# Kernel tuning notes

Measured on AMD Instinct MI355X. Metric: run time of the kernel, lower is better.

Reference implementation:

```python
import jax, jax.numpy as jnp
import numpy as np

BINS = 8
EPS = 1e-12  # torch F.normalize default eps


def _pairwise_scores(matf):
    # torch: input1[a,b]=matf[b]; transpose(0,1)->matf[a]; transpose(-2,-1)->matf[a]^T [M,F]
    # matmul with input1[a,b]=matf[b] -> scores[a,b] = matf[a]^T @ matf[b], shape [M,M]
    bs, F, M = matf.shape
    s = jnp.einsum('afm,bfn->abmn', matf, matf)  # [bs, bs, M, M]
    return s.reshape(bs * bs, M * M)


def _histc_rows(x, bins):
    # torch.histc semantics with min=max=0: range = [row.min(), row.max()],
    # values == max land in the last bin.
    mn = jnp.min(x, axis=1, keepdims=True)
    mx = jnp.max(x, axis=1, keepdims=True)
    denom = jnp.where(mx > mn, mx - mn, jnp.ones_like(mx))
    idx = jnp.clip(jnp.floor((x - mn) / denom * bins).astype(jnp.int32), 0, bins - 1)
    nbs = x.shape[0]
    flat = (idx + (jnp.arange(nbs, dtype=jnp.int32) * bins)[:, None]).ravel()
    h = jnp.zeros(nbs * bins, dtype=x.dtype).at[flat].add(1.0)
    return h.reshape(nbs, bins)


def _l2_normalize(h):
    n = jnp.linalg.norm(h, axis=-1, keepdims=True)
    return h / jnp.maximum(n, EPS)


def setup_inputs() -> dict:
    key = jax.random.key(0)
    k1, k2 = jax.random.split(key)
    bs, F, M = 64, 256, 128
    matf1 = jax.random.normal(k1, (bs, F, M), dtype=jnp.float32)
    matf2 = jax.random.normal(k2, (bs, F, M), dtype=jnp.float32)
    return {"matf1": matf1, "matf2": matf2}


def reference(matf1, matf2):
    # scores are .detach()ed in the original; stop_gradient for faithfulness
    scores1 = jax.lax.stop_gradient(_pairwise_scores(matf1))  # [nbs, M*M]
    scores2 = jax.lax.stop_gradient(_pairwise_scores(matf2))
    h1 = _l2_normalize(_histc_rows(scores1, BINS))  # [nbs, 8]
    h2 = _l2_normalize(_histc_rows(scores2, BINS))
    return jnp.concatenate([h1, h2], axis=-1)  # [nbs, 16]
```

## Files before the change

### kernel.cpp

```cpp
#include <hip/hip_runtime.h>
#include <math.h>

#define BS 64
#define F  256
#define M  128
#define MF (M * F)
#define NTILE 528

typedef unsigned short u16;
typedef _Float16 f16x8 __attribute__((ext_vector_type(8)));
typedef float    f32x16 __attribute__((ext_vector_type(16)));

__global__ __launch_bounds__(256) void convert_f16_kernel(
    const float* __restrict__ m1, const float* __restrict__ m2,
    u16* __restrict__ hT)
{
    __shared__ float tile[64 * M];
    const int mat = blockIdx.x >> 6;
    const int b   = blockIdx.x & 63;
    const int f0  = blockIdx.y * 64;
    const float* src = (mat == 0 ? m1 : m2) + (size_t)b * MF + (size_t)f0 * M;
    const int tid = threadIdx.x;

    const float4* g = (const float4*)src;
    float4* s = (float4*)tile;
    #pragma unroll
    for (int i = 0; i < 8; ++i)
        s[tid + i * 256] = g[tid + i * 256];
    __syncthreads();

    const size_t obase = ((size_t)(mat * BS + b) * 32 + (f0 >> 3)) * 1024;
    #pragma unroll
    for (int it = 0; it < 4; ++it) {
        const int idx = it * 256 + tid;
        const int f8l = idx >> 7;
        const int m   = idx & 127;
        u16 hh[8] __attribute__((aligned(16)));
        #pragma unroll
        for (int j = 0; j < 8; ++j) {
            const float x = tile[(f8l * 8 + j) * M + m];
            const _Float16 h = (_Float16)x;
            hh[j] = __builtin_bit_cast(u16, h);
        }
        *(uint4*)&hT[obase + (size_t)idx * 8] = *(const uint4*)hh;
    }
}


#define SLOAD(S) {                                    \
    const u16* sp = srcp + (S) * 8192;                \
    sr0 = *(const uint4*)(sp);                        \
    sr1 = *(const uint4*)(sp + 1024);                 \
    sr2 = *(const uint4*)(sp + 2048);                 \
    sr3 = *(const uint4*)(sp + 3072);                 \
    sr4 = *(const uint4*)(sp + 4096);                 \
    sr5 = *(const uint4*)(sp + 5120);                 \
    sr6 = *(const uint4*)(sp + 6144);                 \
    sr7 = *(const uint4*)(sp + 7168);                 \
}

#define SWRITE(BUF) {                                 \
    u16* dp = &lds[dstb + (BUF)];                     \
    *(uint4*)(dp)        = sr0;                       \
    *(uint4*)(dp + 1024) = sr1;                       \
    *(uint4*)(dp + 2048) = sr2;                       \
    *(uint4*)(dp + 3072) = sr3;                       \
    *(uint4*)(dp + 4096) = sr4;                       \
    *(uint4*)(dp + 5120) = sr5;                       \
    *(uint4*)(dp + 6144) = sr6;                       \
    *(uint4*)(dp + 7168) = sr7;                       \
}

#define MFMA_SLICE(BUF) {                                                                             \
    __builtin_amdgcn_s_setprio(1);                                                                    \
    _Pragma("unroll")                                                                                 \
    for (int ITl = 0; ITl < 2; ++ITl) {                                                               \
        _Pragma("unroll")                                                                             \
        for (int kk = 0; kk < 2; ++kk) {                                                              \
            const int base = (BUF) + ITl * 4096 + kk * 2048;                                          \
            f16x8 af[4], bf[2];                                                                       \
            _Pragma("unroll")                                                                         \
            for (int t = 0; t < 4; ++t)                                                               \
                af[t] = *(const f16x8*)&lds[base + aoffW + t * 256];                                  \
            bf[0] = *(const f16x8*)&lds[base + boffW];                                                \
            bf[1] = *(const f16x8*)&lds[base + boffW + 256];                                          \
            _Pragma("unroll")                                                                         \
            for (int ti = 0; ti < 4; ++ti) {                                                          \
                acc[ti][0] = __builtin_amdgcn_mfma_f32_32x32x16_f16(af[ti], bf[0], acc[ti][0], 0, 0, 0); \
                acc[ti][1] = __builtin_amdgcn_mfma_f32_32x32x16_f16(af[ti], bf[1], acc[ti][1], 0, 0, 0); \
            }                                                                                         \
        }                                                                                             \
    }                                                                                                 \
    __builtin_amdgcn_s_setprio(0);                                                                    \
}

__global__ __launch_bounds__(512, 2) void gram_hist_mfma(
    const u16* __restrict__ hT, float* __restrict__ out)
{
    __shared__ u16 lds[4 * 2 * 8192];
    __shared__ float smin[8], smax[8];
    __shared__ int hist[4][8];

    const int tid  = threadIdx.x;
    const int lane = tid & 63;
    const int w    = tid >> 6;

    if (tid < 32) hist[tid >> 3][tid & 7] = 0;

    int x = blockIdx.x;
    x = (x & 7) * 66 + (x >> 3);
    int tt = x, ta = 0, cnt = 32;
    while (tt >= cnt) { tt -= cnt; ++ta; cnt = 32 - ta; }
    const int tb  = ta + tt;
    const int mat = blockIdx.y;

    const int m  = w >> 1;
    const int c  = w & 1;
    const int l31   = lane & 31;
    const int lhalf = lane >> 5;

    const int srow = tid >> 7;
    const int tl   = tid & 127;
    const int rsel = (srow < 2) ? (2 * ta + srow) : (2 * tb + (srow - 2));
    const u16* srcp = hT + (size_t)(mat * BS + rsel) * MF + tl * 8;
    const int dstb = srow * 16384 + tl * 8;

    const int aoffW = (m >> 1) * 16384 + lhalf * 1024 + l31 * 8;
    const int boffW = (2 + (m & 1)) * 16384 + lhalf * 1024 + c * 512 + l31 * 8;

    f32x16 acc[4][2];
    #pragma unroll
    for (int ti = 0; ti < 4; ++ti)
        #pragma unroll
        for (int u = 0; u < 2; ++u)
            #pragma unroll
            for (int r = 0; r < 16; ++r) acc[ti][u][r] = 0.0f;

    uint4 sr0, sr1, sr2, sr3, sr4, sr5, sr6, sr7;

    SLOAD(0); SWRITE(0);
    __syncthreads();

    SLOAD(1);
    MFMA_SLICE(0);
    __builtin_amdgcn_sched_barrier(0);
    SWRITE(8192);
    __syncthreads();

    SLOAD(2);
    MFMA_SLICE(8192);
    __builtin_amdgcn_sched_barrier(0);
    SWRITE(0);
    __syncthreads();

    SLOAD(3);
    MFMA_SLICE(0);
    __builtin_amdgcn_sched_barrier(0);
    SWRITE(8192);
    __syncthreads();

    MFMA_SLICE(8192);

    float vmin = acc[0][0][0], vmax = vmin;
    #pragma unroll
    for (int ti = 0; ti < 4; ++ti)
        #pragma unroll
        for (int u = 0; u < 2; ++u)
            #pragma unroll
            for (int r = 0; r < 16; ++r) {
                vmin = fminf(vmin, acc[ti][u][r]);
                vmax = fmaxf(vmax, acc[ti][u][r]);
            }
    #pragma unroll
    for (int off = 1; off < 64; off <<= 1) {
        vmin = fminf(vmin, __shfl_xor(vmin, off, 64));
        vmax = fmaxf(vmax, __shfl_xor(vmax, off, 64));
    }
    if (lane == 0) { smin[w] = vmin; smax[w] = vmax; }
    __syncthreads();
    const float pmn = fminf(smin[m * 2], smin[m * 2 + 1]);
    const float pmx = fmaxf(smax[m * 2], smax[m * 2 + 1]);
    const float denom = (pmx > pmn) ? (pmx - pmn) : 1.0f;
    const float scale = 8.0f / denom;
    const float bias  = -pmn * scale;

    unsigned w0 = 0, w1 = 0;
    #pragma unroll
    for (int ti = 0; ti < 4; ++ti)
        #pragma unroll
        for (int u = 0; u < 2; ++u)
            #pragma unroll
            for (int r = 0; r < 16; ++r) {
                const float t = fmaf(acc[ti][u][r], scale, bias);
                int k = (int)t;
                k = k > 7 ? 7 : k;
                const unsigned inc = 1u << ((k & 3) * 8);
                if (k < 4) w0 += inc; else w1 += inc;
            }
    unsigned e0 = (w0 & 0xFFu)         | (((w0 >> 8)  & 0xFFu) << 16);
    unsigned e1 = ((w0 >> 16) & 0xFFu) | (((w0 >> 24) & 0xFFu) << 16);
    unsigned e2 = (w1 & 0xFFu)         | (((w1 >> 8)  & 0xFFu) << 16);
    unsigned e3 = ((w1 >> 16) & 0xFFu) | (((w1 >> 24) & 0xFFu) << 16);
    #pragma unroll
    for (int off = 32; off > 0; off >>= 1) {
        e0 += __shfl_down(e0, off, 64);
        e1 += __shfl_down(e1, off, 64);
        e2 += __shfl_down(e2, off, 64);
        e3 += __shfl_down(e3, off, 64);
    }
    if (lane == 0) {
        atomicAdd(&hist[m][0], (int)(e0 & 0xFFFFu)); atomicAdd(&hist[m][1], (int)(e0 >> 16));
        atomicAdd(&hist[m][2], (int)(e1 & 0xFFFFu)); atomicAdd(&hist[m][3], (int)(e1 >> 16));
        atomicAdd(&hist[m][4], (int)(e2 & 0xFFFFu)); atomicAdd(&hist[m][5], (int)(e2 >> 16));
        atomicAdd(&hist[m][6], (int)(e3 & 0xFFFFu)); atomicAdd(&hist[m][7], (int)(e3 >> 16));
    }
    __syncthreads();

    if (c == 0 && lane < 8) {
        float ss = 0.0f;
        #pragma unroll
        for (int k = 0; k < 8; ++k) {
            const float cc = (float)hist[m][k];
            ss += cc * cc;
        }
        const float nrm = fmaxf(sqrtf(ss), 1e-12f);
        const float v = (float)hist[m][lane] / nrm;
        const int A = 2 * ta + (m >> 1);
        const int B = 2 * tb + (m & 1);
        out[((size_t)A * BS + B) * 16 + mat * 8 + lane] = v;
        if (A != B)
            out[((size_t)B * BS + A) * 16 + mat * 8 + lane] = v;
    }
}

extern "C" void kernel_launch(void* const* d_in, const int* in_sizes, int n_in,
                              void* d_out, int out_size, void* d_ws, size_t ws_size,
                              hipStream_t stream) {
    const float* m1 = (const float*)d_in[0];
    const float* m2 = (const float*)d_in[1];
    float* out = (float*)d_out;

    u16* hT = (u16*)d_ws;

    convert_f16_kernel<<<dim3(128, 4), 256, 0, stream>>>(m1, m2, hT);
    gram_hist_mfma<<<dim3(NTILE, 2), 512, 0, stream>>>(hT, out);
}
```

Before: 127.9 us.

## Use direct global-to-LDS loads with 1024-thread blocks and finer K pipeline

Replaces the register-staged global loads and LDS writes with global_load_lds direct-to-LDS transfers. Doubles the block to 16 waves, each computing a 64x64 sub-tile. Halves the K-slice size and uses an 8-stage double-buffered loop. The grid is flattened so the XCD id picks the matrix and tile group. This cuts register pressure and staging instructions, at the cost of more barriers per block and smaller per-wave MFMA work.

```diff
diff --git a/kernel.cpp b/kernel.cpp
--- a/kernel.cpp
+++ b/kernel.cpp
@@ -5,11 +5,14 @@
 #define F  256
 #define M  128
 #define MF (M * F)
-#define NTILE 528
+#define NT2 528
 
 typedef unsigned short u16;
 typedef _Float16 f16x8 __attribute__((ext_vector_type(8)));
 typedef float    f32x16 __attribute__((ext_vector_type(16)));
+
+typedef const __attribute__((address_space(1))) void gas_t;
+typedef __attribute__((address_space(3))) void las_t;
 
 __global__ __launch_bounds__(256) void convert_f16_kernel(
     const float* __restrict__ m1, const float* __restrict__ m2,
@@ -47,58 +50,38 @@
 }
 
 
-#define SLOAD(S) {                                    \
-    const u16* sp = srcp + (S) * 8192;                \
-    sr0 = *(const uint4*)(sp);                        \
-    sr1 = *(const uint4*)(sp + 1024);                 \
-    sr2 = *(const uint4*)(sp + 2048);                 \
-    sr3 = *(const uint4*)(sp + 3072);                 \
-    sr4 = *(const uint4*)(sp + 4096);                 \
-    sr5 = *(const uint4*)(sp + 5120);                 \
-    sr6 = *(const uint4*)(sp + 6144);                 \
-    sr7 = *(const uint4*)(sp + 7168);                 \
-}
-
-#define SWRITE(BUF) {                                 \
-    u16* dp = &lds[dstb + (BUF)];                     \
-    *(uint4*)(dp)        = sr0;                       \
-    *(uint4*)(dp + 1024) = sr1;                       \
-    *(uint4*)(dp + 2048) = sr2;                       \
-    *(uint4*)(dp + 3072) = sr3;                       \
-    *(uint4*)(dp + 4096) = sr4;                       \
-    *(uint4*)(dp + 5120) = sr5;                       \
-    *(uint4*)(dp + 6144) = sr6;                       \
-    *(uint4*)(dp + 7168) = sr7;                       \
-}
-
-#define MFMA_SLICE(BUF) {                                                                             \
-    __builtin_amdgcn_s_setprio(1);                                                                    \
-    _Pragma("unroll")                                                                                 \
-    for (int ITl = 0; ITl < 2; ++ITl) {                                                               \
-        _Pragma("unroll")                                                                             \
-        for (int kk = 0; kk < 2; ++kk) {                                                              \
-            const int base = (BUF) + ITl * 4096 + kk * 2048;                                          \
-            f16x8 af[4], bf[2];                                                                       \
-            _Pragma("unroll")                                                                         \
-            for (int t = 0; t < 4; ++t)                                                               \
-                af[t] = *(const f16x8*)&lds[base + aoffW + t * 256];                                  \
-            bf[0] = *(const f16x8*)&lds[base + boffW];                                                \
-            bf[1] = *(const f16x8*)&lds[base + boffW + 256];                                          \
-            _Pragma("unroll")                                                                         \
-            for (int ti = 0; ti < 4; ++ti) {                                                          \
-                acc[ti][0] = __builtin_amdgcn_mfma_f32_32x32x16_f16(af[ti], bf[0], acc[ti][0], 0, 0, 0); \
-                acc[ti][1] = __builtin_amdgcn_mfma_f32_32x32x16_f16(af[ti], bf[1], acc[ti][1], 0, 0, 0); \
-            }                                                                                         \
-        }                                                                                             \
-    }                                                                                                 \
-    __builtin_amdgcn_s_setprio(0);                                                                    \
-}
-
-__global__ __launch_bounds__(512, 2) void gram_hist_mfma(
+#define GLOAD(S, BUF) {                                                       \
+    const u16* g0 = srow + (S) * 4096 + j0 * 512 + lane * 8;                  \
+    const u16* g1 = srow + (S) * 4096 + j1 * 512 + lane * 8;                  \
+    __builtin_amdgcn_global_load_lds((gas_t*)g0,                              \
+        (las_t*)&lds[ldst0 + (BUF)], 16, 0, 0);                               \
+    __builtin_amdgcn_global_load_lds((gas_t*)g1,                              \
+        (las_t*)&lds[ldst1 + (BUF)], 16, 0, 0);                               \
+}
+
+#define MFMA_SLICE(BUF) {                                                     \
+    __builtin_amdgcn_s_setprio(1);                                            \
+    _Pragma("unroll")                                                         \
+    for (int kk = 0; kk < 2; ++kk) {                                          \
+        const int ab = ra * 8192 + (BUF) + kk * 2048 + aoffb;                 \
+        const int bb = rb * 8192 + (BUF) + kk * 2048 + boffb;                 \
+        const f16x8 a0 = *(const f16x8*)&lds[ab];                             \
+        const f16x8 a1 = *(const f16x8*)&lds[ab + 256];                       \
+        const f16x8 b0 = *(const f16x8*)&lds[bb];                             \
+        const f16x8 b1 = *(const f16x8*)&lds[bb + 256];                       \
+        acc[0][0] = __builtin_amdgcn_mfma_f32_32x32x16_f16(a0, b0, acc[0][0], 0, 0, 0); \
+        acc[0][1] = __builtin_amdgcn_mfma_f32_32x32x16_f16(a0, b1, acc[0][1], 0, 0, 0); \
+        acc[1][0] = __builtin_amdgcn_mfma_f32_32x32x16_f16(a1, b0, acc[1][0], 0, 0, 0); \
+        acc[1][1] = __builtin_amdgcn_mfma_f32_32x32x16_f16(a1, b1, acc[1][1], 0, 0, 0); \
+    }                                                                         \
+    __builtin_amdgcn_s_setprio(0);                                            \
+}
+
+__global__ __launch_bounds__(1024, 4) void gram_hist_mfma(
     const u16* __restrict__ hT, float* __restrict__ out)
 {
-    __shared__ u16 lds[4 * 2 * 8192];
-    __shared__ float smin[8], smax[8];
+    __shared__ u16 lds[4 * 2 * 4096];
+    __shared__ float smin[16], smax[16];
     __shared__ int hist[4][8];
 
     const int tid  = threadIdx.x;
@@ -107,69 +90,63 @@
 
     if (tid < 32) hist[tid >> 3][tid & 7] = 0;
 
-    int x = blockIdx.x;
-    x = (x & 7) * 66 + (x >> 3);
-    int tt = x, ta = 0, cnt = 32;
-    while (tt >= cnt) { tt -= cnt; ++ta; cnt = 32 - ta; }
-    const int tb  = ta + tt;
-    const int mat = blockIdx.y;
-
-    const int m  = w >> 1;
-    const int c  = w & 1;
+    const int bid = blockIdx.x;
+    const int xcd = bid & 7;
+    const int mat = xcd >> 2;
+    int p = (xcd & 3) * 132 + (bid >> 3);
+    int ta = 0;
+    { int cnt = 32; while (p >= cnt) { p -= cnt; ++ta; cnt = 32 - ta; } }
+    const int tb = ta + p;
+
+    const int m  = w >> 2;
+    const int q  = w & 3;
+    const int qr = q >> 1;
+    const int qc = q & 1;
     const int l31   = lane & 31;
     const int lhalf = lane >> 5;
 
-    const int srow = tid >> 7;
-    const int tl   = tid & 127;
-    const int rsel = (srow < 2) ? (2 * ta + srow) : (2 * tb + (srow - 2));
-    const u16* srcp = hT + (size_t)(mat * BS + rsel) * MF + tl * 8;
-    const int dstb = srow * 16384 + tl * 8;
-
-    const int aoffW = (m >> 1) * 16384 + lhalf * 1024 + l31 * 8;
-    const int boffW = (2 + (m & 1)) * 16384 + lhalf * 1024 + c * 512 + l31 * 8;
-
-    f32x16 acc[4][2];
-    #pragma unroll
-    for (int ti = 0; ti < 4; ++ti)
+    const int k0  = w * 2;
+    const int r_s = k0 >> 3;
+    const int rowsel = (r_s < 2) ? (2 * ta + r_s) : (2 * tb + (r_s - 2));
+    const u16* srow = hT + (size_t)(mat * BS + rowsel) * MF;
+    const int j0 = k0 & 7, j1 = (k0 + 1) & 7;
+    const int ldst0 = r_s * 8192 + j0 * 512;
+    const int ldst1 = r_s * 8192 + j1 * 512;
+
+    const int ra = m >> 1;
+    const int rb = 2 + (m & 1);
+    const int aoffb = lhalf * 1024 + qr * 512 + l31 * 8;
+    const int boffb = lhalf * 1024 + qc * 512 + l31 * 8;
+
+    f32x16 acc[2][2];
+    #pragma unroll
+    for (int t = 0; t < 2; ++t)
         #pragma unroll
         for (int u = 0; u < 2; ++u)
             #pragma unroll
-            for (int r = 0; r < 16; ++r) acc[ti][u][r] = 0.0f;
-
-    uint4 sr0, sr1, sr2, sr3, sr4, sr5, sr6, sr7;
-
-    SLOAD(0); SWRITE(0);
-    __syncthreads();
-
-    SLOAD(1);
-    MFMA_SLICE(0);
-    __builtin_amdgcn_sched_barrier(0);
-    SWRITE(8192);
-    __syncthreads();
-
-    SLOAD(2);
-    MFMA_SLICE(8192);
-    __builtin_amdgcn_sched_barrier(0);
-    SWRITE(0);
-    __syncthreads();
-
-    SLOAD(3);
-    MFMA_SLICE(0);
-    __builtin_amdgcn_sched_barrier(0);
-    SWRITE(8192);
-    __syncthreads();
-
-    MFMA_SLICE(8192);
+            for (int r = 0; r < 16; ++r) acc[t][u][r] = 0.0f;
+
+    GLOAD(0, 0);
+    __syncthreads();
+
+    #pragma unroll
+    for (int s = 0; s < 8; ++s) {
+        const int cur = (s & 1) * 4096;
+        const int alt = cur ^ 4096;
+        if (s < 7) GLOAD(s + 1, alt);
+        MFMA_SLICE(cur);
+        __syncthreads();
+    }
 
     float vmin = acc[0][0][0], vmax = vmin;
     #pragma unroll
-    for (int ti = 0; ti < 4; ++ti)
+    for (int t = 0; t < 2; ++t)
         #pragma unroll
         for (int u = 0; u < 2; ++u)
             #pragma unroll
             for (int r = 0; r < 16; ++r) {
-                vmin = fminf(vmin, acc[ti][u][r]);
-                vmax = fmaxf(vmax, acc[ti][u][r]);
+                vmin = fminf(vmin, acc[t][u][r]);
+                vmax = fmaxf(vmax, acc[t][u][r]);
             }
     #pragma unroll
     for (int off = 1; off < 64; off <<= 1) {
@@ -178,21 +155,24 @@
     }
     if (lane == 0) { smin[w] = vmin; smax[w] = vmax; }
     __syncthreads();
-    const float pmn = fminf(smin[m * 2], smin[m * 2 + 1]);
-    const float pmx = fmaxf(smax[m * 2], smax[m * 2 + 1]);
+    const int m4 = m * 4;
+    const float pmn = fminf(fminf(smin[m4], smin[m4 + 1]),
+                            fminf(smin[m4 + 2], smin[m4 + 3]));
+    const float pmx = fmaxf(fmaxf(smax[m4], smax[m4 + 1]),
+                            fmaxf(smax[m4 + 2], smax[m4 + 3]));
     const float denom = (pmx > pmn) ? (pmx - pmn) : 1.0f;
     const float scale = 8.0f / denom;
     const float bias  = -pmn * scale;
 
     unsigned w0 = 0, w1 = 0;
     #pragma unroll
-    for (int ti = 0; ti < 4; ++ti)
+    for (int t = 0; t < 2; ++t)
         #pragma unroll
         for (int u = 0; u < 2; ++u)
             #pragma unroll
             for (int r = 0; r < 16; ++r) {
-                const float t = fmaf(acc[ti][u][r], scale, bias);
-                int k = (int)t;
+                const float tv = fmaf(acc[t][u][r], scale, bias);
+                int k = (int)tv;
                 k = k > 7 ? 7 : k;
                 const unsigned inc = 1u << ((k & 3) * 8);
                 if (k < 4) w0 += inc; else w1 += inc;
@@ -216,7 +196,7 @@
     }
     __syncthreads();
 
-    if (c == 0 && lane < 8) {
+    if (q == 0 && lane < 8) {
         float ss = 0.0f;
         #pragma unroll
         for (int k = 0; k < 8; ++k) {
@@ -243,5 +223,5 @@
     u16* hT = (u16*)d_ws;
 
     convert_f16_kernel<<<dim3(128, 4), 256, 0, stream>>>(m1, m2, hT);
-    gram_hist_mfma<<<dim3(NTILE, 2), 512, 0, stream>>>(hT, out);
-}
+    gram_hist_mfma<<<2 * NT2, 1024, 0, stream>>>(hT, out);
+}
```

Result: slower. 133.8 us (+4.6%).
